# Performance work log

Measured on AMD Instinct MI355X. Metric: run time of the kernel, lower is better.

Reference implementation:

```python
import jax, jax.numpy as jnp
import numpy as np

B = 512          # batch
D = 2048         # num_variables / leaf folds of a balanced binary region graph
K = 32           # num_units (sum/input units per fold)


def setup_inputs() -> dict:
    key = jax.random.key(0)
    k1, k2, k3 = jax.random.split(key, 3)
    # input-layer log-densities per (variable-region, unit): [B, D, K]
    x = jax.random.normal(k1, (B, D, K), dtype=jnp.float32)
    # packed per-fold CP mixing weights for all inner layers: sum_l F_l = D-1 folds
    weights = jax.random.uniform(k2, (D - 1, K, K), dtype=jnp.float32,
                                 minval=0.01, maxval=1.0)  # positive (monotonic)
    # packed fold_idx bookkeeping: layer l gathers children (2f, 2f+1) of prev layer
    idx_list = []
    F = D
    while F > 1:
        F //= 2
        idx_list.append(np.arange(2 * F, dtype=np.int32).reshape(F, 2))
    fold_idx = jnp.asarray(np.concatenate(idx_list, axis=0))  # [D-1, 2]
    # out-mixture logits over the root's K units (num_classes = 1)
    mix_logw = jax.random.normal(k3, (K,), dtype=jnp.float32)
    return {"x": x, "weights": weights, "fold_idx": fold_idx, "mix_logw": mix_logw}


def _log_matmul_exp(a, w):
    # a: [B, F, K] log-values; w: [F, K, Kout] positive weights
    # y_j = log sum_i exp(a_i) * w_ij, computed stably via max-subtraction
    m = jnp.max(a, axis=-1, keepdims=True)
    y = jnp.einsum('bfi,fij->bfj', jnp.exp(a - m), w)
    return jnp.log(y) + m


def reference(x, weights, fold_idx, mix_logw):
    # DAG evaluation: gather via fold_idx, CP layer = log-product of the two
    # gathered children followed by a per-fold log-linear mixture.
    out = x                      # [B, F, K]
    off = 0
    F = x.shape[1]
    while F > 1:                 # static Python loop over log2(D)=11 layers
        F //= 2
        idx = fold_idx[off:off + F]            # [F, 2] child indices (static slice)
        inp = out[:, idx, :]                   # gather -> [B, F, 2, K]
        prod = inp[:, :, 0, :] + inp[:, :, 1, :]   # log-space product node
        out = _log_matmul_exp(prod, weights[off:off + F])  # sum node -> [B, F, K]
        off += F
    # Born real path: outputs = 2 * real(log amp), then MonotonicMixtureLayer
    flat = 2.0 * out[:, 0, :]                  # [B, K]
    logw = jax.nn.log_softmax(mix_logw)        # normalized mixture weights
    return jax.nn.logsumexp(flat + logw[None, :], axis=-1)  # [B]
```

## Files before the change

### kernel.cpp

```cpp
#include <hip/hip_runtime.h>

#define KK 32
#define BATCH 512
#define DD 2048
#define ESTRIDE 36
#define NUNIT (KK * BATCH)

__device__ __forceinline__ void node8L(const float p8[8],
                                       const float* __restrict__ Wt,
                                       float* __restrict__ e_lds,
                                       float* __restrict__ pm_lds, int jg,
                                       int lane, int j0, float o8[8]) {
  const float a0 = fmaxf(p8[0], p8[1]), a1 = fmaxf(p8[2], p8[3]);
  const float a2 = fmaxf(p8[4], p8[5]), a3 = fmaxf(p8[6], p8[7]);
  pm_lds[jg * 65 + lane] = fmaxf(fmaxf(a0, a1), fmaxf(a2, a3));
  __syncthreads();
  const float m = fmaxf(fmaxf(pm_lds[lane], pm_lds[65 + lane]),
                        fmaxf(pm_lds[130 + lane], pm_lds[195 + lane]));

  float4* ew = reinterpret_cast<float4*>(e_lds + lane * ESTRIDE + j0);
  ew[0] = make_float4(__expf(p8[0] - m), __expf(p8[1] - m),
                      __expf(p8[2] - m), __expf(p8[3] - m));
  ew[1] = make_float4(__expf(p8[4] - m), __expf(p8[5] - m),
                      __expf(p8[6] - m), __expf(p8[7] - m));
  __syncthreads();

  const float4* er = reinterpret_cast<const float4*>(e_lds + lane * ESTRIDE);
  const float4* WL = reinterpret_cast<const float4*>(Wt) + (j0 >> 2);

  float acc[8];
#pragma unroll
  for (int j = 0; j < 8; ++j) acc[j] = 0.0f;

#pragma unroll 1
  for (int q = 0; q < 8; ++q) {
    const float4 ev = er[q];
    const int i0 = 4 * q;
    const float4 wa0 = WL[(i0 + 0) * 8], wa1 = WL[(i0 + 0) * 8 + 1];
    const float4 wb0 = WL[(i0 + 1) * 8], wb1 = WL[(i0 + 1) * 8 + 1];
    const float4 wc0 = WL[(i0 + 2) * 8], wc1 = WL[(i0 + 2) * 8 + 1];
    const float4 wd0 = WL[(i0 + 3) * 8], wd1 = WL[(i0 + 3) * 8 + 1];
    acc[0] = fmaf(ev.x, wa0.x, acc[0]); acc[1] = fmaf(ev.x, wa0.y, acc[1]);
    acc[2] = fmaf(ev.x, wa0.z, acc[2]); acc[3] = fmaf(ev.x, wa0.w, acc[3]);
    acc[4] = fmaf(ev.x, wa1.x, acc[4]); acc[5] = fmaf(ev.x, wa1.y, acc[5]);
    acc[6] = fmaf(ev.x, wa1.z, acc[6]); acc[7] = fmaf(ev.x, wa1.w, acc[7]);
    acc[0] = fmaf(ev.y, wb0.x, acc[0]); acc[1] = fmaf(ev.y, wb0.y, acc[1]);
    acc[2] = fmaf(ev.y, wb0.z, acc[2]); acc[3] = fmaf(ev.y, wb0.w, acc[3]);
    acc[4] = fmaf(ev.y, wb1.x, acc[4]); acc[5] = fmaf(ev.y, wb1.y, acc[5]);
    acc[6] = fmaf(ev.y, wb1.z, acc[6]); acc[7] = fmaf(ev.y, wb1.w, acc[7]);
    acc[0] = fmaf(ev.z, wc0.x, acc[0]); acc[1] = fmaf(ev.z, wc0.y, acc[1]);
    acc[2] = fmaf(ev.z, wc0.z, acc[2]); acc[3] = fmaf(ev.z, wc0.w, acc[3]);
    acc[4] = fmaf(ev.z, wc1.x, acc[4]); acc[5] = fmaf(ev.z, wc1.y, acc[5]);
    acc[6] = fmaf(ev.z, wc1.z, acc[6]); acc[7] = fmaf(ev.z, wc1.w, acc[7]);
    acc[0] = fmaf(ev.w, wd0.x, acc[0]); acc[1] = fmaf(ev.w, wd0.y, acc[1]);
    acc[2] = fmaf(ev.w, wd0.z, acc[2]); acc[3] = fmaf(ev.w, wd0.w, acc[3]);
    acc[4] = fmaf(ev.w, wd1.x, acc[4]); acc[5] = fmaf(ev.w, wd1.y, acc[5]);
    acc[6] = fmaf(ev.w, wd1.z, acc[6]); acc[7] = fmaf(ev.w, wd1.w, acc[7]);
  }
#pragma unroll
  for (int j = 0; j < 8; ++j) o8[j] = __logf(acc[j]) + m;
}

__device__ __forceinline__ void addv8(const float a[8], const float b[8],
                                      float o[8]) {
#pragma unroll
  for (int j = 0; j < 8; ++j) o[j] = a[j] + b[j];
}

__device__ __forceinline__ void pairload_x(const float* __restrict__ xb,
                                           int leaf, int j0, float p[8]) {
  const float4* u = reinterpret_cast<const float4*>(xb + leaf * KK + j0);
  const float4* v = reinterpret_cast<const float4*>(xb + (leaf + 1) * KK + j0);
  const float4 u0 = u[0], u1 = u[1], v0 = v[0], v1 = v[1];
  p[0] = u0.x + v0.x; p[1] = u0.y + v0.y; p[2] = u0.z + v0.z; p[3] = u0.w + v0.w;
  p[4] = u1.x + v1.x; p[5] = u1.y + v1.y; p[6] = u1.z + v1.z; p[7] = u1.w + v1.w;
}

__device__ __forceinline__ void pairload_n(const float* __restrict__ in,
                                           int node, int j0, int b, float p[8]) {
  const float* p0 = in + (size_t)node * NUNIT + (size_t)j0 * BATCH + b;
  const float* p1 = p0 + NUNIT;
#pragma unroll
  for (int k = 0; k < 8; ++k) p[k] = p0[k * BATCH] + p1[k * BATCH];
}

__global__ __launch_bounds__(256, 4) void kern1(const float* __restrict__ x,
                                                const float* __restrict__ W,
                                                float* __restrict__ o) {
  __shared__ __align__(16) float W_lds[7 * KK * KK];
  __shared__ __align__(16) float e_lds[64 * ESTRIDE];
  __shared__ float pm_lds[4 * 65];
  const int tid = threadIdx.x;
  const int lane = tid & 63;
  const int jg = __builtin_amdgcn_readfirstlane(tid >> 6);
  const int j0 = jg * 8;
  const int b = blockIdx.y * 64 + lane;
  const int chunk = blockIdx.x;
  const int c4 = chunk * 4, c2 = chunk * 2;
  const float* xb = x + (size_t)b * (DD * KK) + (size_t)chunk * 8 * KK;

  const float4* W4 = reinterpret_cast<const float4*>(W);
  float4* WL4 = reinterpret_cast<float4*>(W_lds);
  WL4[tid]            = W4[(size_t)(c4 + 0) * 256 + tid];
  WL4[256 + tid]      = W4[(size_t)(c4 + 1) * 256 + tid];
  WL4[512 + tid]      = W4[(size_t)(1024 + c2 + 0) * 256 + tid];
  WL4[768 + tid]      = W4[(size_t)(c4 + 2) * 256 + tid];
  WL4[1024 + tid]     = W4[(size_t)(c4 + 3) * 256 + tid];
  WL4[1280 + tid]     = W4[(size_t)(1024 + c2 + 1) * 256 + tid];
  WL4[1536 + tid]     = W4[(size_t)(1536 + chunk) * 256 + tid];

  float p[8], a0[8], a1[8], b0[8], b1[8], o8[8];

  pairload_x(xb, 0, j0, p);
  node8L(p, W_lds + 0 * 1024, e_lds, pm_lds, jg, lane, j0, a0);
  pairload_x(xb, 2, j0, p);
  node8L(p, W_lds + 1 * 1024, e_lds, pm_lds, jg, lane, j0, a1);
  addv8(a0, a1, p);
  node8L(p, W_lds + 2 * 1024, e_lds, pm_lds, jg, lane, j0, b0);
  pairload_x(xb, 4, j0, p);
  node8L(p, W_lds + 3 * 1024, e_lds, pm_lds, jg, lane, j0, a0);
  pairload_x(xb, 6, j0, p);
  node8L(p, W_lds + 4 * 1024, e_lds, pm_lds, jg, lane, j0, a1);
  addv8(a0, a1, p);
  node8L(p, W_lds + 5 * 1024, e_lds, pm_lds, jg, lane, j0, b1);
  addv8(b0, b1, p);
  node8L(p, W_lds + 6 * 1024, e_lds, pm_lds, jg, lane, j0, o8);

#pragma unroll
  for (int j = 0; j < 8; ++j)
    o[(size_t)chunk * NUNIT + (size_t)(j0 + j) * BATCH + b] = o8[j];
}

__global__ __launch_bounds__(256, 4) void kernL(const float* __restrict__ in,
                                                const float* __restrict__ W,
                                                float* __restrict__ o,
                                                int woff) {
  __shared__ __align__(16) float W_lds[KK * KK];
  __shared__ __align__(16) float e_lds[64 * ESTRIDE];
  __shared__ float pm_lds[4 * 65];
  const int tid = threadIdx.x;
  const int lane = tid & 63;
  const int jg = __builtin_amdgcn_readfirstlane(tid >> 6);
  const int j0 = jg * 8;
  const int b = blockIdx.y * 64 + lane;
  const int n = blockIdx.x;

  reinterpret_cast<float4*>(W_lds)[tid] =
      reinterpret_cast<const float4*>(W)[(size_t)(woff + n) * 256 + tid];

  float p[8], o8[8];
  pairload_n(in, 2 * n, j0, b, p);
  node8L(p, W_lds, e_lds, pm_lds, jg, lane, j0, o8);

#pragma unroll
  for (int j = 0; j < 8; ++j)
    o[(size_t)n * NUNIT + (size_t)(j0 + j) * BATCH + b] = o8[j];
}

__global__ __launch_bounds__(256, 4) void kernF(const float* __restrict__ in,
                                                const float* __restrict__ W,
                                                const float* __restrict__ mixw,
                                                float* __restrict__ out) {
  __shared__ __align__(16) float W_lds[3 * KK * KK];
  __shared__ __align__(16) float e_lds[64 * ESTRIDE];
  __shared__ float pm_lds[4 * 65];
  const int tid = threadIdx.x;
  const int lane = tid & 63;
  const int jg = __builtin_amdgcn_readfirstlane(tid >> 6);
  const int j0 = jg * 8;
  const int b = blockIdx.y * 64 + lane;

  const float4* W4 = reinterpret_cast<const float4*>(W);
  float4* WL4 = reinterpret_cast<float4*>(W_lds);
  WL4[tid]       = W4[(size_t)2044 * 256 + tid];
  WL4[256 + tid] = W4[(size_t)2045 * 256 + tid];
  WL4[512 + tid] = W4[(size_t)2046 * 256 + tid];

  float p[8], a0[8], a1[8], o8[8];
  pairload_n(in, 0, j0, b, p);
  node8L(p, W_lds + 0 * 1024, e_lds, pm_lds, jg, lane, j0, a0);
  pairload_n(in, 2, j0, b, p);
  node8L(p, W_lds + 1 * 1024, e_lds, pm_lds, jg, lane, j0, a1);
  addv8(a0, a1, p);
  node8L(p, W_lds + 2 * 1024, e_lds, pm_lds, jg, lane, j0, o8);

  float wv32[KK];
#pragma unroll
  for (int i = 0; i < KK; ++i) wv32[i] = mixw[i];
  float t[KK];
#pragma unroll
  for (int i = 0; i < KK; ++i) t[i] = wv32[i];
#pragma unroll
  for (int s = KK / 2; s >= 1; s >>= 1)
#pragma unroll
    for (int i = 0; i < s; ++i) t[i] = fmaxf(t[i], t[i + s]);
  const float wm = t[0];
  float ws = 0.0f;
#pragma unroll
  for (int i = 0; i < KK; ++i) ws += __expf(wv32[i] - wm);
  const float lsew = __logf(ws) + wm;

  float t8[8];
#pragma unroll
  for (int j = 0; j < 8; ++j) t8[j] = 2.0f * o8[j] + (wv32[j0 + j] - lsew);
  const float c0 = fmaxf(t8[0], t8[1]), c1 = fmaxf(t8[2], t8[3]);
  const float c2 = fmaxf(t8[4], t8[5]), c3 = fmaxf(t8[6], t8[7]);
  __syncthreads();
  pm_lds[jg * 65 + lane] = fmaxf(fmaxf(c0, c1), fmaxf(c2, c3));
  __syncthreads();
  const float m2 = fmaxf(fmaxf(pm_lds[lane], pm_lds[65 + lane]),
                         fmaxf(pm_lds[130 + lane], pm_lds[195 + lane]));
  float ss = 0.0f;
#pragma unroll
  for (int j = 0; j < 8; ++j) ss += __expf(t8[j] - m2);
  __syncthreads();
  pm_lds[jg * 65 + lane] = ss;
  __syncthreads();
  if (jg == 0) {
    const float s4 = (pm_lds[lane] + pm_lds[65 + lane]) +
                     (pm_lds[130 + lane] + pm_lds[195 + lane]);
    out[b] = __logf(s4) + m2;
  }
}

extern "C" void kernel_launch(void* const* d_in, const int* in_sizes, int n_in,
                              void* d_out, int out_size, void* d_ws,
                              size_t ws_size, hipStream_t stream) {
  const float* x = (const float*)d_in[0];
  const float* W = (const float*)d_in[1];
  const float* mixw = (const float*)d_in[3];
  float* out = (float*)d_out;

  float* A = (float*)d_ws;
  float* Bb = A + (size_t)256 * NUNIT;

  kern1<<<dim3(256, 8), 256, 0, stream>>>(x, W, A);
  kernL<<<dim3(128, 8), 256, 0, stream>>>(A, W, Bb, 1792);
  kernL<<<dim3(64, 8), 256, 0, stream>>>(Bb, W, A, 1920);
  kernL<<<dim3(32, 8), 256, 0, stream>>>(A, W, Bb, 1984);
  kernL<<<dim3(16, 8), 256, 0, stream>>>(Bb, W, A, 2016);
  kernL<<<dim3(8, 8), 256, 0, stream>>>(A, W, Bb, 2032);
  kernL<<<dim3(4, 8), 256, 0, stream>>>(Bb, W, A, 2040);
  kernF<<<dim3(1, 8), 256, 0, stream>>>(A, W, mixw, out);
}
```

Measured before the change: 248.8 us.

## Fuse tree levels pairwise and batch sibling nodes to halve barriers

Replaces the six single-level kernels with three kernels that each evaluate two tree levels, so there are fewer launches and fewer global round-trips for intermediates. Sibling nodes are also processed together through a paired node routine that shares the two barriers per node and interleaves two independent FMA chains. kern1 now preloads all four leaf pairs up front. The cost is more LDS per block and more registers, which may reduce occupancy, and the later levels launch fewer blocks.

```diff
diff --git a/kernel.cpp b/kernel.cpp
--- a/kernel.cpp
+++ b/kernel.cpp
@@ -6,32 +6,107 @@
 #define ESTRIDE 36
 #define NUNIT (KK * BATCH)
 
+__device__ __forceinline__ float max8(const float p[8]) {
+  const float a0 = fmaxf(p[0], p[1]), a1 = fmaxf(p[2], p[3]);
+  const float a2 = fmaxf(p[4], p[5]), a3 = fmaxf(p[6], p[7]);
+  return fmaxf(fmaxf(a0, a1), fmaxf(a2, a3));
+}
+__device__ __forceinline__ float max4pm(const float* pm, int lane) {
+  return fmaxf(fmaxf(pm[lane], pm[65 + lane]),
+               fmaxf(pm[130 + lane], pm[195 + lane]));
+}
+__device__ __forceinline__ void write_e(float* __restrict__ E, int lane,
+                                        int j0, const float p[8], float m) {
+  float4* ew = reinterpret_cast<float4*>(E + lane * ESTRIDE + j0);
+  ew[0] = make_float4(__expf(p[0] - m), __expf(p[1] - m), __expf(p[2] - m),
+                      __expf(p[3] - m));
+  ew[1] = make_float4(__expf(p[4] - m), __expf(p[5] - m), __expf(p[6] - m),
+                      __expf(p[7] - m));
+}
+__device__ __forceinline__ void addv8(const float a[8], const float b[8],
+                                      float o[8]) {
+#pragma unroll
+  for (int j = 0; j < 8; ++j) o[j] = a[j] + b[j];
+}
+
+#define MAC8(acc, e, w0, w1)                                   \
+  acc[0] = fmaf(e, w0.x, acc[0]); acc[1] = fmaf(e, w0.y, acc[1]); \
+  acc[2] = fmaf(e, w0.z, acc[2]); acc[3] = fmaf(e, w0.w, acc[3]); \
+  acc[4] = fmaf(e, w1.x, acc[4]); acc[5] = fmaf(e, w1.y, acc[5]); \
+  acc[6] = fmaf(e, w1.z, acc[6]); acc[7] = fmaf(e, w1.w, acc[7]);
+
+__device__ __forceinline__ void node8_pair(
+    const float pa[8], const float pb[8], const float* __restrict__ Wa,
+    const float* __restrict__ Wb, float* __restrict__ Ea,
+    float* __restrict__ Eb, float* __restrict__ pm, int jg, int lane, int j0,
+    float oa[8], float ob[8]) {
+  pm[jg * 65 + lane] = max8(pa);
+  pm[260 + jg * 65 + lane] = max8(pb);
+  __syncthreads();
+  const float ma = max4pm(pm, lane);
+  const float mb = max4pm(pm + 260, lane);
+  write_e(Ea, lane, j0, pa, ma);
+  write_e(Eb, lane, j0, pb, mb);
+  __syncthreads();
+
+  const float4* era = reinterpret_cast<const float4*>(Ea + lane * ESTRIDE);
+  const float4* erb = reinterpret_cast<const float4*>(Eb + lane * ESTRIDE);
+  const float4* WLa = reinterpret_cast<const float4*>(Wa) + (j0 >> 2);
+  const float4* WLb = reinterpret_cast<const float4*>(Wb) + (j0 >> 2);
+
+  float acca[8], accb[8];
+#pragma unroll
+  for (int j = 0; j < 8; ++j) { acca[j] = 0.0f; accb[j] = 0.0f; }
+
+#pragma unroll 1
+  for (int q = 0; q < 8; ++q) {
+    const float4 eva = era[q];
+    const float4 evb = erb[q];
+    const int i0 = 4 * q;
+    {
+      const float4 w0 = WLa[(i0 + 0) * 8], w1 = WLa[(i0 + 0) * 8 + 1];
+      const float4 v0 = WLb[(i0 + 0) * 8], v1 = WLb[(i0 + 0) * 8 + 1];
+      MAC8(acca, eva.x, w0, w1) MAC8(accb, evb.x, v0, v1)
+    }
+    {
+      const float4 w0 = WLa[(i0 + 1) * 8], w1 = WLa[(i0 + 1) * 8 + 1];
+      const float4 v0 = WLb[(i0 + 1) * 8], v1 = WLb[(i0 + 1) * 8 + 1];
+      MAC8(acca, eva.y, w0, w1) MAC8(accb, evb.y, v0, v1)
+    }
+    {
+      const float4 w0 = WLa[(i0 + 2) * 8], w1 = WLa[(i0 + 2) * 8 + 1];
+      const float4 v0 = WLb[(i0 + 2) * 8], v1 = WLb[(i0 + 2) * 8 + 1];
+      MAC8(acca, eva.z, w0, w1) MAC8(accb, evb.z, v0, v1)
+    }
+    {
+      const float4 w0 = WLa[(i0 + 3) * 8], w1 = WLa[(i0 + 3) * 8 + 1];
+      const float4 v0 = WLb[(i0 + 3) * 8], v1 = WLb[(i0 + 3) * 8 + 1];
+      MAC8(acca, eva.w, w0, w1) MAC8(accb, evb.w, v0, v1)
+    }
+  }
+#pragma unroll
+  for (int j = 0; j < 8; ++j) {
+    oa[j] = __logf(acca[j]) + ma;
+    ob[j] = __logf(accb[j]) + mb;
+  }
+}
+
 __device__ __forceinline__ void node8L(const float p8[8],
                                        const float* __restrict__ Wt,
-                                       float* __restrict__ e_lds,
-                                       float* __restrict__ pm_lds, int jg,
+                                       float* __restrict__ E,
+                                       float* __restrict__ pm, int jg,
                                        int lane, int j0, float o8[8]) {
-  const float a0 = fmaxf(p8[0], p8[1]), a1 = fmaxf(p8[2], p8[3]);
-  const float a2 = fmaxf(p8[4], p8[5]), a3 = fmaxf(p8[6], p8[7]);
-  pm_lds[jg * 65 + lane] = fmaxf(fmaxf(a0, a1), fmaxf(a2, a3));
-  __syncthreads();
-  const float m = fmaxf(fmaxf(pm_lds[lane], pm_lds[65 + lane]),
-                        fmaxf(pm_lds[130 + lane], pm_lds[195 + lane]));
-
-  float4* ew = reinterpret_cast<float4*>(e_lds + lane * ESTRIDE + j0);
-  ew[0] = make_float4(__expf(p8[0] - m), __expf(p8[1] - m),
-                      __expf(p8[2] - m), __expf(p8[3] - m));
-  ew[1] = make_float4(__expf(p8[4] - m), __expf(p8[5] - m),
-                      __expf(p8[6] - m), __expf(p8[7] - m));
-  __syncthreads();
-
-  const float4* er = reinterpret_cast<const float4*>(e_lds + lane * ESTRIDE);
+  pm[jg * 65 + lane] = max8(p8);
+  __syncthreads();
+  const float m = max4pm(pm, lane);
+  write_e(E, lane, j0, p8, m);
+  __syncthreads();
+
+  const float4* er = reinterpret_cast<const float4*>(E + lane * ESTRIDE);
   const float4* WL = reinterpret_cast<const float4*>(Wt) + (j0 >> 2);
-
   float acc[8];
 #pragma unroll
   for (int j = 0; j < 8; ++j) acc[j] = 0.0f;
-
 #pragma unroll 1
   for (int q = 0; q < 8; ++q) {
     const float4 ev = er[q];
@@ -40,31 +115,11 @@
     const float4 wb0 = WL[(i0 + 1) * 8], wb1 = WL[(i0 + 1) * 8 + 1];
     const float4 wc0 = WL[(i0 + 2) * 8], wc1 = WL[(i0 + 2) * 8 + 1];
     const float4 wd0 = WL[(i0 + 3) * 8], wd1 = WL[(i0 + 3) * 8 + 1];
-    acc[0] = fmaf(ev.x, wa0.x, acc[0]); acc[1] = fmaf(ev.x, wa0.y, acc[1]);
-    acc[2] = fmaf(ev.x, wa0.z, acc[2]); acc[3] = fmaf(ev.x, wa0.w, acc[3]);
-    acc[4] = fmaf(ev.x, wa1.x, acc[4]); acc[5] = fmaf(ev.x, wa1.y, acc[5]);
-    acc[6] = fmaf(ev.x, wa1.z, acc[6]); acc[7] = fmaf(ev.x, wa1.w, acc[7]);
-    acc[0] = fmaf(ev.y, wb0.x, acc[0]); acc[1] = fmaf(ev.y, wb0.y, acc[1]);
-    acc[2] = fmaf(ev.y, wb0.z, acc[2]); acc[3] = fmaf(ev.y, wb0.w, acc[3]);
-    acc[4] = fmaf(ev.y, wb1.x, acc[4]); acc[5] = fmaf(ev.y, wb1.y, acc[5]);
-    acc[6] = fmaf(ev.y, wb1.z, acc[6]); acc[7] = fmaf(ev.y, wb1.w, acc[7]);
-    acc[0] = fmaf(ev.z, wc0.x, acc[0]); acc[1] = fmaf(ev.z, wc0.y, acc[1]);
-    acc[2] = fmaf(ev.z, wc0.z, acc[2]); acc[3] = fmaf(ev.z, wc0.w, acc[3]);
-    acc[4] = fmaf(ev.z, wc1.x, acc[4]); acc[5] = fmaf(ev.z, wc1.y, acc[5]);
-    acc[6] = fmaf(ev.z, wc1.z, acc[6]); acc[7] = fmaf(ev.z, wc1.w, acc[7]);
-    acc[0] = fmaf(ev.w, wd0.x, acc[0]); acc[1] = fmaf(ev.w, wd0.y, acc[1]);
-    acc[2] = fmaf(ev.w, wd0.z, acc[2]); acc[3] = fmaf(ev.w, wd0.w, acc[3]);
-    acc[4] = fmaf(ev.w, wd1.x, acc[4]); acc[5] = fmaf(ev.w, wd1.y, acc[5]);
-    acc[6] = fmaf(ev.w, wd1.z, acc[6]); acc[7] = fmaf(ev.w, wd1.w, acc[7]);
+    MAC8(acc, ev.x, wa0, wa1) MAC8(acc, ev.y, wb0, wb1)
+    MAC8(acc, ev.z, wc0, wc1) MAC8(acc, ev.w, wd0, wd1)
   }
 #pragma unroll
   for (int j = 0; j < 8; ++j) o8[j] = __logf(acc[j]) + m;
-}
-
-__device__ __forceinline__ void addv8(const float a[8], const float b[8],
-                                      float o[8]) {
-#pragma unroll
-  for (int j = 0; j < 8; ++j) o[j] = a[j] + b[j];
 }
 
 __device__ __forceinline__ void pairload_x(const float* __restrict__ xb,
@@ -88,8 +143,9 @@
                                                 const float* __restrict__ W,
                                                 float* __restrict__ o) {
   __shared__ __align__(16) float W_lds[7 * KK * KK];
-  __shared__ __align__(16) float e_lds[64 * ESTRIDE];
-  __shared__ float pm_lds[4 * 65];
+  __shared__ __align__(16) float Ea[64 * ESTRIDE];
+  __shared__ __align__(16) float Eb[64 * ESTRIDE];
+  __shared__ float pm[2 * 260];
   const int tid = threadIdx.x;
   const int lane = tid & 63;
   const int jg = __builtin_amdgcn_readfirstlane(tid >> 6);
@@ -97,47 +153,50 @@
   const int b = blockIdx.y * 64 + lane;
   const int chunk = blockIdx.x;
   const int c4 = chunk * 4, c2 = chunk * 2;
-  const float* xb = x + (size_t)b * (DD * KK) + (size_t)chunk * 8 * KK;
 
   const float4* W4 = reinterpret_cast<const float4*>(W);
   float4* WL4 = reinterpret_cast<float4*>(W_lds);
-  WL4[tid]            = W4[(size_t)(c4 + 0) * 256 + tid];
-  WL4[256 + tid]      = W4[(size_t)(c4 + 1) * 256 + tid];
-  WL4[512 + tid]      = W4[(size_t)(1024 + c2 + 0) * 256 + tid];
-  WL4[768 + tid]      = W4[(size_t)(c4 + 2) * 256 + tid];
-  WL4[1024 + tid]     = W4[(size_t)(c4 + 3) * 256 + tid];
-  WL4[1280 + tid]     = W4[(size_t)(1024 + c2 + 1) * 256 + tid];
-  WL4[1536 + tid]     = W4[(size_t)(1536 + chunk) * 256 + tid];
-
-  float p[8], a0[8], a1[8], b0[8], b1[8], o8[8];
-
-  pairload_x(xb, 0, j0, p);
-  node8L(p, W_lds + 0 * 1024, e_lds, pm_lds, jg, lane, j0, a0);
-  pairload_x(xb, 2, j0, p);
-  node8L(p, W_lds + 1 * 1024, e_lds, pm_lds, jg, lane, j0, a1);
-  addv8(a0, a1, p);
-  node8L(p, W_lds + 2 * 1024, e_lds, pm_lds, jg, lane, j0, b0);
-  pairload_x(xb, 4, j0, p);
-  node8L(p, W_lds + 3 * 1024, e_lds, pm_lds, jg, lane, j0, a0);
-  pairload_x(xb, 6, j0, p);
-  node8L(p, W_lds + 4 * 1024, e_lds, pm_lds, jg, lane, j0, a1);
-  addv8(a0, a1, p);
-  node8L(p, W_lds + 5 * 1024, e_lds, pm_lds, jg, lane, j0, b1);
-  addv8(b0, b1, p);
-  node8L(p, W_lds + 6 * 1024, e_lds, pm_lds, jg, lane, j0, o8);
+  WL4[tid]        = W4[(size_t)(c4 + 0) * 256 + tid];
+  WL4[256 + tid]  = W4[(size_t)(c4 + 1) * 256 + tid];
+  WL4[512 + tid]  = W4[(size_t)(c4 + 2) * 256 + tid];
+  WL4[768 + tid]  = W4[(size_t)(c4 + 3) * 256 + tid];
+  WL4[1024 + tid] = W4[(size_t)(1024 + c2 + 0) * 256 + tid];
+  WL4[1280 + tid] = W4[(size_t)(1024 + c2 + 1) * 256 + tid];
+  WL4[1536 + tid] = W4[(size_t)(1536 + chunk) * 256 + tid];
+
+  const float* xb = x + (size_t)b * (DD * KK) + (size_t)chunk * 8 * KK;
+  float pA0[8], pB0[8], pA1[8], pB1[8];
+  pairload_x(xb, 0, j0, pA0);
+  pairload_x(xb, 2, j0, pB0);
+  pairload_x(xb, 4, j0, pA1);
+  pairload_x(xb, 6, j0, pB1);
+
+  float n0[8], n1[8], n2[8], n3[8], m0[8], m1[8], o8[8], p[8], q[8];
+
+  node8_pair(pA0, pB0, W_lds + 0 * 1024, W_lds + 1 * 1024, Ea, Eb, pm, jg,
+             lane, j0, n0, n1);
+  node8_pair(pA1, pB1, W_lds + 2 * 1024, W_lds + 3 * 1024, Ea, Eb, pm, jg,
+             lane, j0, n2, n3);
+  addv8(n0, n1, p);
+  addv8(n2, n3, q);
+  node8_pair(p, q, W_lds + 4 * 1024, W_lds + 5 * 1024, Ea, Eb, pm, jg, lane,
+             j0, m0, m1);
+  addv8(m0, m1, p);
+  node8L(p, W_lds + 6 * 1024, Ea, pm, jg, lane, j0, o8);
 
 #pragma unroll
   for (int j = 0; j < 8; ++j)
     o[(size_t)chunk * NUNIT + (size_t)(j0 + j) * BATCH + b] = o8[j];
 }
 
-__global__ __launch_bounds__(256, 4) void kernL(const float* __restrict__ in,
+__global__ __launch_bounds__(256, 4) void kernT(const float* __restrict__ in,
                                                 const float* __restrict__ W,
-                                                float* __restrict__ o,
-                                                int woff) {
-  __shared__ __align__(16) float W_lds[KK * KK];
-  __shared__ __align__(16) float e_lds[64 * ESTRIDE];
-  __shared__ float pm_lds[4 * 65];
+                                                float* __restrict__ o, int lo,
+                                                int hi) {
+  __shared__ __align__(16) float W_lds[3 * KK * KK];
+  __shared__ __align__(16) float Ea[64 * ESTRIDE];
+  __shared__ __align__(16) float Eb[64 * ESTRIDE];
+  __shared__ float pm[2 * 260];
   const int tid = threadIdx.x;
   const int lane = tid & 63;
   const int jg = __builtin_amdgcn_readfirstlane(tid >> 6);
@@ -145,12 +204,18 @@
   const int b = blockIdx.y * 64 + lane;
   const int n = blockIdx.x;
 
-  reinterpret_cast<float4*>(W_lds)[tid] =
-      reinterpret_cast<const float4*>(W)[(size_t)(woff + n) * 256 + tid];
-
-  float p[8], o8[8];
-  pairload_n(in, 2 * n, j0, b, p);
-  node8L(p, W_lds, e_lds, pm_lds, jg, lane, j0, o8);
+  const float4* W4 = reinterpret_cast<const float4*>(W);
+  float4* WL4 = reinterpret_cast<float4*>(W_lds);
+  WL4[tid]       = W4[(size_t)(lo + 2 * n + 0) * 256 + tid];
+  WL4[256 + tid] = W4[(size_t)(lo + 2 * n + 1) * 256 + tid];
+  WL4[512 + tid] = W4[(size_t)(hi + n) * 256 + tid];
+
+  float pa[8], pb[8], r0[8], r1[8], p[8], o8[8];
+  pairload_n(in, 4 * n + 0, j0, b, pa);
+  pairload_n(in, 4 * n + 2, j0, b, pb);
+  node8_pair(pa, pb, W_lds, W_lds + 1024, Ea, Eb, pm, jg, lane, j0, r0, r1);
+  addv8(r0, r1, p);
+  node8L(p, W_lds + 2048, Ea, pm, jg, lane, j0, o8);
 
 #pragma unroll
   for (int j = 0; j < 8; ++j)
@@ -162,8 +227,9 @@
                                                 const float* __restrict__ mixw,
                                                 float* __restrict__ out) {
   __shared__ __align__(16) float W_lds[3 * KK * KK];
-  __shared__ __align__(16) float e_lds[64 * ESTRIDE];
-  __shared__ float pm_lds[4 * 65];
+  __shared__ __align__(16) float Ea[64 * ESTRIDE];
+  __shared__ __align__(16) float Eb[64 * ESTRIDE];
+  __shared__ float pm[2 * 260];
   const int tid = threadIdx.x;
   const int lane = tid & 63;
   const int jg = __builtin_amdgcn_readfirstlane(tid >> 6);
@@ -176,13 +242,12 @@
   WL4[256 + tid] = W4[(size_t)2045 * 256 + tid];
   WL4[512 + tid] = W4[(size_t)2046 * 256 + tid];
 
-  float p[8], a0[8], a1[8], o8[8];
-  pairload_n(in, 0, j0, b, p);
-  node8L(p, W_lds + 0 * 1024, e_lds, pm_lds, jg, lane, j0, a0);
-  pairload_n(in, 2, j0, b, p);
-  node8L(p, W_lds + 1 * 1024, e_lds, pm_lds, jg, lane, j0, a1);
-  addv8(a0, a1, p);
-  node8L(p, W_lds + 2 * 1024, e_lds, pm_lds, jg, lane, j0, o8);
+  float pa[8], pb[8], r0[8], r1[8], p[8], o8[8];
+  pairload_n(in, 0, j0, b, pa);
+  pairload_n(in, 2, j0, b, pb);
+  node8_pair(pa, pb, W_lds, W_lds + 1024, Ea, Eb, pm, jg, lane, j0, r0, r1);
+  addv8(r0, r1, p);
+  node8L(p, W_lds + 2048, Ea, pm, jg, lane, j0, o8);
 
   float wv32[KK];
 #pragma unroll
@@ -203,22 +268,18 @@
   float t8[8];
 #pragma unroll
   for (int j = 0; j < 8; ++j) t8[j] = 2.0f * o8[j] + (wv32[j0 + j] - lsew);
-  const float c0 = fmaxf(t8[0], t8[1]), c1 = fmaxf(t8[2], t8[3]);
-  const float c2 = fmaxf(t8[4], t8[5]), c3 = fmaxf(t8[6], t8[7]);
-  __syncthreads();
-  pm_lds[jg * 65 + lane] = fmaxf(fmaxf(c0, c1), fmaxf(c2, c3));
-  __syncthreads();
-  const float m2 = fmaxf(fmaxf(pm_lds[lane], pm_lds[65 + lane]),
-                         fmaxf(pm_lds[130 + lane], pm_lds[195 + lane]));
+  __syncthreads();
+  pm[jg * 65 + lane] = max8(t8);
+  __syncthreads();
+  const float m2 = max4pm(pm, lane);
   float ss = 0.0f;
 #pragma unroll
   for (int j = 0; j < 8; ++j) ss += __expf(t8[j] - m2);
   __syncthreads();
-  pm_lds[jg * 65 + lane] = ss;
+  pm[jg * 65 + lane] = ss;
   __syncthreads();
   if (jg == 0) {
-    const float s4 = (pm_lds[lane] + pm_lds[65 + lane]) +
-                     (pm_lds[130 + lane] + pm_lds[195 + lane]);
+    const float s4 = (pm[lane] + pm[65 + lane]) + (pm[130 + lane] + pm[195 + lane]);
     out[b] = __logf(s4) + m2;
   }
 }
@@ -235,11 +296,8 @@
   float* Bb = A + (size_t)256 * NUNIT;
 
   kern1<<<dim3(256, 8), 256, 0, stream>>>(x, W, A);
-  kernL<<<dim3(128, 8), 256, 0, stream>>>(A, W, Bb, 1792);
-  kernL<<<dim3(64, 8), 256, 0, stream>>>(Bb, W, A, 1920);
-  kernL<<<dim3(32, 8), 256, 0, stream>>>(A, W, Bb, 1984);
-  kernL<<<dim3(16, 8), 256, 0, stream>>>(Bb, W, A, 2016);
-  kernL<<<dim3(8, 8), 256, 0, stream>>>(A, W, Bb, 2032);
-  kernL<<<dim3(4, 8), 256, 0, stream>>>(Bb, W, A, 2040);
-  kernF<<<dim3(1, 8), 256, 0, stream>>>(A, W, mixw, out);
-}
+  kernT<<<dim3(64, 8), 256, 0, stream>>>(A, W, Bb, 1792, 1920);
+  kernT<<<dim3(16, 8), 256, 0, stream>>>(Bb, W, A, 1984, 2016);
+  kernT<<<dim3(4, 8), 256, 0, stream>>>(A, W, Bb, 2032, 2040);
+  kernF<<<dim3(1, 8), 256, 0, stream>>>(Bb, W, mixw, out);
+}
```

New measurement: 243.3 us. 1.02x faster.
